# Optimization experiments

Measured on AMD Instinct MI355X. Metric: run time of the kernel, lower is better.

## Reference

```python
import jax, jax.numpy as jnp
import numpy as np

POOL = 7          # pool_size
RES = 42          # ROIS_resolution
CH = 2048         # backbone output channels (Xception)
GCN_DIM = 256     # gcn_outfeat_dim (== gat_outfeat_dim after head split, heads=1)
HEADS = 1
GAT_CH = 256
ALPHA = 0.1       # APPNP teleport
EPS = 1e-3        # keras BatchNormalization epsilon
CHUNKS = CH // GCN_DIM            # 8 channel chunks per ROI
CNODES = CHUNKS * POOL * POOL     # 392 intra-graph nodes


def _rois():
    # fixed ROI boxes (x, y, w, h) on the 42x42 upsampled map:
    # 3x3 grid of 14x14 cells + two horizontal halves + full image
    c = RES // 3
    r = [(x * c, y * c, c, c) for y in range(3) for x in range(3)]
    r += [(0, 0, RES, RES // 2), (0, RES // 2, RES, RES // 2), (0, 0, RES, RES)]
    return r

ROIS = _rois()
NUM_ROIS = len(ROIS)  # 12


def _gcn_adj(n):
    # spektral GCNConv.preprocess on all-ones adjacency: D^-1/2 (A + I) D^-1/2
    a = np.ones((n, n), np.float32) + np.eye(n, dtype=np.float32)
    d = a.sum(1)
    return jnp.asarray(a / np.sqrt(np.outer(d, d)))

A_INTRA = _gcn_adj(CNODES)        # (392, 392)
A_INTER = _gcn_adj(NUM_ROIS + 1)  # (13, 13)


def _appnp(x, a, w, b):
    # APPNPConv, propagations=1, sigmoid MLP: (1-a)*A@m + a*m
    m = jax.nn.sigmoid(x @ w + b)
    return (1.0 - ALPHA) * jnp.einsum('nm,...mf->...nf', a, m) + ALPHA * m


def _gat(x, a, k, a_self, a_neigh, b):
    # GATConv._call_dense (inference: dropout off); a has add_self_loops folded in
    xp = jnp.einsum('...ni,iho->...nho', x, k)          # (...,N,H,C)
    s = jnp.einsum('...nhi,iho->...nho', xp, a_self)    # (...,N,H,1)
    t = jnp.einsum('...nhi,iho->...nho', xp, a_neigh)   # (...,N,H,1)
    coef = s + jnp.swapaxes(t, -3, -1)                  # (...,N,H,N)
    coef = jax.nn.leaky_relu(coef, 0.2)
    mask = jnp.where(a == 0.0, -1e10, 0.0)              # (N,N) (all-connected here)
    coef = jax.nn.softmax(coef + mask[:, None, :], axis=-1)
    out = jnp.einsum('...nhm,...mhi->...nhi', coef, xp)
    out = out.reshape(out.shape[:-2] + (HEADS * GAT_CH,))  # concat heads
    return jax.nn.elu(out + b)


def _gnn_block(x, a, aw, ab, gk, gs, gn, gb):
    h = _appnp(x, a, aw, ab) + x
    return _gat(h, a, gk, gs, gn, gb) + h


def setup_inputs() -> dict:
    key = jax.random.key(0)
    ks = jax.random.split(key, 8)
    s = 0.05
    return {
        'base_out': jax.random.normal(ks[0], (8, POOL, POOL, CH), jnp.float32),
        'appnp_w': jax.random.normal(ks[1], (GCN_DIM, GCN_DIM), jnp.float32) * s,
        'appnp_b': jnp.zeros((GCN_DIM,), jnp.float32),
        'gat_kernel': jax.random.normal(ks[2], (GCN_DIM, HEADS, GAT_CH), jnp.float32) * s,
        'gat_attn_self': jax.random.normal(ks[3], (GAT_CH, HEADS, 1), jnp.float32) * s,
        'gat_attn_neighs': jax.random.normal(ks[4], (GAT_CH, HEADS, 1), jnp.float32) * s,
        'gat_bias': jnp.zeros((HEADS * GAT_CH,), jnp.float32),
        'pool_feat_w': jax.random.normal(ks[5], (GCN_DIM, 2 * GCN_DIM), jnp.float32) * s,
        'pool_feat_b': jnp.zeros((2 * GCN_DIM,), jnp.float32),
        'pool_attn_w': jax.random.normal(ks[6], (GCN_DIM, 2 * GCN_DIM), jnp.float32) * s,
        'pool_attn_b': jnp.zeros((2 * GCN_DIM,), jnp.float32),
        'bn_gamma': jnp.ones((2 * GCN_DIM,), jnp.float32),
        'bn_beta': jnp.zeros((2 * GCN_DIM,), jnp.float32),
        'bn_mean': jnp.zeros((2 * GCN_DIM,), jnp.float32),
        'bn_var': jnp.ones((2 * GCN_DIM,), jnp.float32),
        'dense_w': jax.random.normal(ks[7], (2 * GCN_DIM, 200), jnp.float32) * s,
        'dense_b': jnp.zeros((200,), jnp.float32),
    }


def reference(base_out, appnp_w, appnp_b, gat_kernel, gat_attn_self, gat_attn_neighs,
              gat_bias, pool_feat_w, pool_feat_b, pool_attn_w, pool_attn_b,
              bn_gamma, bn_beta, bn_mean, bn_var, dense_w, dense_b):
    B = base_out.shape[0]
    # upsample backbone features to ROI resolution
    x0 = jax.image.resize(base_out, (B, RES, RES, CH), 'bilinear')
    # RoiPoolingConv: crop each static ROI and resize to (POOL, POOL)
    pooled = [jax.image.resize(x0[:, y:y + h, x:x + w, :], (B, POOL, POOL, CH), 'bilinear')
              for (x, y, w, h) in ROIS]
    pooled.append(base_out)  # global node (pool_size == base_out spatial dim)
    rois = jnp.stack(pooled, axis=1)  # (B, R+1, 7, 7, CH)
    # _temp_nodes_transform: split channels into CHUNKS, concat along node axis
    nodes = rois.reshape(B, NUM_ROIS + 1, POOL * POOL, CHUNKS, GCN_DIM)
    nodes = nodes.transpose(0, 1, 3, 2, 4).reshape(B, NUM_ROIS + 1, CNODES, GCN_DIM)
    gnn = (appnp_w, appnp_b, gat_kernel, gat_attn_self, gat_attn_neighs, gat_bias)
    # intra-ROI graphs: 13 independent 392-node graphs (batched over (B, R+1))
    x2_intra = _gnn_block(nodes, A_INTRA, *gnn).reshape(B, (NUM_ROIS + 1) * CNODES, GCN_DIM)
    # inter-ROI graphs: 392 independent 13-node graphs
    xt = nodes.transpose(0, 2, 1, 3)  # (B, CNODES, R+1, GCN_DIM)
    x2_inter = _gnn_block(xt, A_INTER, *gnn).reshape(B, CNODES * (NUM_ROIS + 1), GCN_DIM)
    x2 = jnp.concatenate([x2_intra, x2_inter], axis=1)  # (B, 10192, 256)
    # GlobalAttentionPool(512)
    feat = x2 @ pool_feat_w + pool_feat_b
    gate = jax.nn.sigmoid(x2 @ pool_attn_w + pool_attn_b)
    xf = jnp.sum(gate * feat, axis=1)  # (B, 512)
    # BatchNorm (inference) + softmax classifier
    xn = (xf - bn_mean) / jnp.sqrt(bn_var + EPS) * bn_gamma + bn_beta
    return jax.nn.softmax(xn @ dense_w + dense_b, axis=-1)
```

## Files before the change

### kernel.cpp

```cpp
#include <hip/hip_runtime.h>
#include <math.h>


typedef __attribute__((ext_vector_type(8))) short bf16x8;
typedef __attribute__((ext_vector_type(4))) float f32x4;

#define MFMA16x32(a, b, c) __builtin_amdgcn_mfma_f32_16x16x32_bf16((a), (b), (c), 0, 0, 0)

__device__ __forceinline__ float sigmoidf_(float x) { return 1.0f / (1.0f + expf(-x)); }
__device__ __forceinline__ float leakyf_(float x) { return x >= 0.0f ? x : 0.2f * x; }
__device__ __forceinline__ float eluf_(float x) { return x > 0.0f ? x : expm1f(x); }
__device__ __forceinline__ short f2bf(float f) {
  unsigned u = __builtin_bit_cast(unsigned, f);
  unsigned r = u + 0x7fffu + ((u >> 16) & 1u);
  return (short)(r >> 16);
}
__device__ __forceinline__ float bf2f(short s) {
  unsigned u = ((unsigned)(unsigned short)s) << 16;
  return __builtin_bit_cast(float, u);
}
__device__ __forceinline__ f32x4 fzero4() {
  f32x4 z;
  #pragma unroll
  for (int i = 0; i < 4; ++i) z[i] = 0.0f;
  return z;
}

__global__ void wtab_k(float* __restrict__ wtab) {
  const int RX[12] = {0,14,28, 0,14,28, 0,14,28, 0, 0, 0};
  const int RY[12] = {0, 0, 0,14,14,14,28,28,28, 0,21, 0};
  const int RW[12] = {14,14,14,14,14,14,14,14,14,42,42,42};
  const int RH[12] = {14,14,14,14,14,14,14,14,14,21,21,42};
  for (int e = threadIdx.x; e < 13 * 2 * 49; e += blockDim.x) {
    const int roi = e / 98;
    const int rest = e % 98;
    const int axis = rest / 49;
    const int o = (rest % 49) / 7;
    const int ib = rest % 7;
    float wout;
    if (roi == 12) {
      wout = (o == ib) ? 1.0f : 0.0f;
    } else {
      const int start = axis ? RX[roi] : RY[roi];
      const int len = axis ? RW[roi] : RH[roi];
      const float s = (float)len / 7.0f;
      const float oc = (o + 0.5f) * s - 0.5f;
      float wsum = 0.0f, dot = 0.0f;
      for (int j = 0; j < len; ++j) {
        float w = 1.0f - fabsf((float)j - oc) / s;
        if (w <= 0.0f) continue;
        wsum += w;
        const float ic = ((float)(start + j) + 0.5f) / 6.0f - 0.5f;
        const float fl = floorf(ic);
        const int ia = (int)fl;
        const float fr = ic - fl;
        int c0 = ia;     if (c0 < 0) c0 = 0; if (c0 > 6) c0 = 6;
        int c1 = ia + 1; if (c1 < 0) c1 = 0; if (c1 > 6) c1 = 6;
        float u = 0.0f;
        if (c0 == ib) u += 1.0f - fr;
        if (c1 == ib) u += fr;
        dot += w * u;
      }
      wout = dot / wsum;
    }
    wtab[e] = wout;
  }
}

__global__ void wcvt_k(const float* __restrict__ src, short* __restrict__ hi,
                       int K, int N) {
  const int idx = blockIdx.x * 256 + threadIdx.x;
  if (idx >= K * N) return;
  const int k = idx / N, n = idx % N;
  hi[(size_t)n * K + k] = f2bf(src[idx]);
}

__global__ void wcvt_pool_k(const float* __restrict__ Wf, const float* __restrict__ Wa,
                            short* __restrict__ BT) {
  const int idx = blockIdx.x * 256 + threadIdx.x;
  if (idx >= 1024 * 256) return;
  const int n = idx >> 8, k = idx & 255;
  const int p = n >> 4, i = n & 15;
  const int sc = ((p >> 1) << 4) + i;
  const float v = (p & 1) ? Wa[(size_t)k * 512 + sc] : Wf[(size_t)k * 512 + sc];
  BT[(size_t)n * 256 + k] = f2bf(v);
}

__global__ void wvec_k(const float* __restrict__ Wk, const float* __restrict__ as,
                       const float* __restrict__ an, float* __restrict__ was,
                       float* __restrict__ wan) {
  const int w = threadIdx.x >> 6, l = threadIdx.x & 63;
  const int row = blockIdx.x * 4 + w;
  const float* p = Wk + (size_t)row * 256;
  float s = 0.0f, t = 0.0f;
  #pragma unroll
  for (int j = 0; j < 4; ++j) {
    const int o = l + j * 64;
    const float v = p[o];
    s = fmaf(v, as[o], s);
    t = fmaf(v, an[o], t);
  }
  #pragma unroll
  for (int off = 32; off; off >>= 1) { s += __shfl_down(s, off); t += __shfl_down(t, off); }
  if (l == 0) { was[row] = s; wan[row] = t; }
}

__global__ __launch_bounds__(256) void nodes_k(const float* __restrict__ base,
                                               const float* __restrict__ wtab,
                                               short* __restrict__ nodes) {
  const int blk = blockIdx.x;
  const int chunk = blk & 7;
  const int br = blk >> 3;
  const int r = br % 13;
  const int b = br / 13;
  const int f = threadIdx.x;
  __shared__ float W49[49][50];
  const float* wv = wtab + (r * 2 + 0) * 49;
  const float* wh = wtab + (r * 2 + 1) * 49;
  for (int e = f; e < 2401; e += 256) {
    const int o = e / 49, in = e % 49;
    W49[o][in] = wv[(o / 7) * 7 + in / 7] * wh[(o % 7) * 7 + in % 7];
  }
  __syncthreads();
  float bv[49];
  const float* bp = base + (size_t)b * 49 * 2048 + chunk * 256 + f;
  #pragma unroll
  for (int in = 0; in < 49; ++in) bv[in] = bp[(size_t)in * 2048];
  const size_t obase = ((size_t)(b * 13 + r) * 392 + chunk * 49) * 256 + f;
  for (int o = 0; o < 49; ++o) {
    float acc = 0.0f;
    #pragma unroll
    for (int in = 0; in < 49; ++in) acc = fmaf(W49[o][in], bv[in], acc);
    nodes[obase + (size_t)o * 256] = f2bf(acc);
  }
}

enum { EP_PLAIN = 0, EP_SIG = 1, EP_POOL = 3 };

template <int EPI>
__global__ __launch_bounds__(256) void gemm_t(
    const short* __restrict__ A, const short* __restrict__ BT,
    const int Kpad, const int nkt, const int Mvalid,
    const float* __restrict__ e0, const float* __restrict__ e1,
    short* __restrict__ Cs, float* __restrict__ xf) {
  const int tid = threadIdx.x;
  const int w = tid >> 6, l = tid & 63;
  const int lr = l & 15, kb = l >> 4;
  const int wr = w >> 1, wc = w & 1;

  int row0, col0, rbase = 0, bseg = 0;
  if constexpr (EPI == EP_POOL) {
    const int bid = blockIdx.x;
    const int eff = (bid & 7) * 640 + (bid >> 3);
    const int mt = eff >> 3, ct = eff & 7;
    row0 = mt * 128; col0 = ct * 128;
    rbase = (mt % 40) * 128;
    bseg = (mt / 40) & 7;
  } else {
    row0 = blockIdx.x * 128; col0 = blockIdx.y * 128;
  }

  __shared__ short As[128][32];
  __shared__ short Bs[128][32];

  const int srow = w * 32 + (l >> 2);
  const int sso = (l & 3) * 8;
  const short* ag0 = A + (size_t)(row0 + srow) * Kpad + sso;
  const short* ag1 = ag0 + (size_t)16 * Kpad;
  const short* bg0 = BT + (size_t)(col0 + srow) * Kpad + sso;
  const short* bg1 = bg0 + (size_t)16 * Kpad;

  f32x4 acc[4][4];
  #pragma unroll
  for (int i = 0; i < 4; ++i)
    #pragma unroll
    for (int j = 0; j < 4; ++j) acc[i][j] = fzero4();

  bf16x8 ra0 = *(const bf16x8*)ag0;
  bf16x8 ra1 = *(const bf16x8*)ag1;
  bf16x8 rb0 = *(const bf16x8*)bg0;
  bf16x8 rb1 = *(const bf16x8*)bg1;

  for (int kt = 0; kt < nkt; ++kt) {
    __syncthreads();
    *(bf16x8*)&As[srow][sso] = ra0;
    *(bf16x8*)&As[srow + 16][sso] = ra1;
    *(bf16x8*)&Bs[srow][sso] = rb0;
    *(bf16x8*)&Bs[srow + 16][sso] = rb1;
    if (kt + 1 < nkt) {
      const int ko = (kt + 1) * 32;
      ra0 = *(const bf16x8*)(ag0 + ko);
      ra1 = *(const bf16x8*)(ag1 + ko);
      rb0 = *(const bf16x8*)(bg0 + ko);
      rb1 = *(const bf16x8*)(bg1 + ko);
    }
    __syncthreads();
    bf16x8 va[4], vb[4];
    #pragma unroll
    for (int i = 0; i < 4; ++i) va[i] = *(const bf16x8*)&As[wr * 64 + i * 16 + lr][kb * 8];
    #pragma unroll
    for (int j = 0; j < 4; ++j) vb[j] = *(const bf16x8*)&Bs[wc * 64 + j * 16 + lr][kb * 8];
    #pragma unroll
    for (int i = 0; i < 4; ++i)
      #pragma unroll
      for (int j = 0; j < 4; ++j) acc[i][j] = MFMA16x32(va[i], vb[j], acc[i][j]);
  }

  if constexpr (EPI == EP_PLAIN || EPI == EP_SIG) {
    #pragma unroll
    for (int j = 0; j < 4; ++j) {
      const int col = col0 + wc * 64 + j * 16 + lr;
      float bs = 0.0f;
      if constexpr (EPI == EP_SIG) bs = e0[col];
      #pragma unroll
      for (int i = 0; i < 4; ++i) {
        const int row = row0 + wr * 64 + i * 16 + kb * 4;
        #pragma unroll
        for (int r = 0; r < 4; ++r) {
          if (row + r < Mvalid) {
            float o = acc[i][j][r];
            if constexpr (EPI == EP_SIG) o = sigmoidf_(o + bs);
            Cs[(size_t)(row + r) * 256 + col] = f2bf(o);
          }
        }
      }
    }
  } else {
    #pragma unroll
    for (int jp = 0; jp < 2; ++jp) {
      const int j = jp * 2;
      const int cg = col0 + wc * 64 + j * 16;
      const int realcol = ((cg >> 5) << 4) + lr;
      const float bfv = e0[realcol], bav = e1[realcol];
      float cs = 0.0f;
      #pragma unroll
      for (int i = 0; i < 4; ++i) {
        const int rl = rbase + wr * 64 + i * 16 + kb * 4;
        #pragma unroll
        for (int r = 0; r < 4; ++r) {
          if (rl + r < 5096) {
            const float fv = acc[i][j][r] + bfv;
            const float gv = acc[i][j + 1][r] + bav;
            cs += sigmoidf_(gv) * fv;
          }
        }
      }
      cs += __shfl_xor(cs, 16);
      cs += __shfl_xor(cs, 32);
      if (l < 16) atomicAdd(&xf[(size_t)bseg * 512 + realcol], cs);
    }
  }
}

__global__ __launch_bounds__(256) void pv_flash_k(
    const short* __restrict__ xpT, const float* __restrict__ sb,
    const float* __restrict__ tb, const float* __restrict__ dinv,
    const float* __restrict__ bias, const short* __restrict__ h,
    short* __restrict__ x2) {
  const int g = blockIdx.z;
  const int rh = blockIdx.y;
  const int ct = blockIdx.x;
  const int tid = threadIdx.x;
  const int w = tid >> 6, l = tid & 63;
  const int lr = l & 15, kb = l >> 4;
  const int wr = w >> 1, wc = w & 1;

  __shared__ short As[128][32];
  __shared__ short Bs[128][32];
  __shared__ float t_s[416];
  __shared__ float red[256];

  for (int i = tid; i < 416; i += 256)
    t_s[i] = (i < 392) ? tb[(size_t)g * 392 + i] : -1e30f;
  __syncthreads();
  float lm = -1e30f;
  for (int i = tid; i < 392; i += 256) lm = fmaxf(lm, t_s[i]);
  red[tid] = lm;
  __syncthreads();
  for (int off = 128; off; off >>= 1) {
    if (tid < off) red[tid] = fmaxf(red[tid], red[tid + off]);
    __syncthreads();
  }
  const float tmax = red[0];

  const int srow = w * 32 + (l >> 2);
  const int sso = (l & 3) * 8;
  const short* bg0 = xpT + ((size_t)g * 256 + ct * 128 + srow) * 448 + sso;
  const short* bg1 = bg0 + (size_t)16 * 448;
  const int bb = g / 13, rr = g % 13;

  for (int rt = 0; rt < 2; ++rt) {
    const int row0 = rh * 256 + rt * 128;
    const int ar0 = row0 + srow, ar1 = row0 + srow + 16;
    const bool v0 = ar0 < 392, v1 = ar1 < 392;
    const float sv0 = v0 ? sb[(size_t)g * 392 + ar0] : 0.0f;
    const float sv1 = v1 ? sb[(size_t)g * 392 + ar1] : 0.0f;
    const float lt0 = leakyf_(sv0 + tmax);
    const float lt1 = leakyf_(sv1 + tmax);

    f32x4 acc[4][4];
    #pragma unroll
    for (int i = 0; i < 4; ++i)
      #pragma unroll
      for (int j = 0; j < 4; ++j) acc[i][j] = fzero4();

    bf16x8 rb0 = *(const bf16x8*)bg0;
    bf16x8 rb1 = *(const bf16x8*)bg1;

    for (int kt = 0; kt < 13; ++kt) {
      __syncthreads();
      *(bf16x8*)&Bs[srow][sso] = rb0;
      *(bf16x8*)&Bs[srow + 16][sso] = rb1;
      {
        const int mb = kt * 32 + sso;
        bf16x8 e0v, e1v;
        #pragma unroll
        for (int i = 0; i < 8; ++i) {
          const float tm = t_s[mb + i];
          e0v[i] = v0 ? f2bf(__expf(leakyf_(sv0 + tm) - lt0)) : (short)0;
          e1v[i] = v1 ? f2bf(__expf(leakyf_(sv1 + tm) - lt1)) : (short)0;
        }
        *(bf16x8*)&As[srow][sso] = e0v;
        *(bf16x8*)&As[srow + 16][sso] = e1v;
      }
      if (kt + 1 < 13) {
        const int ko = (kt + 1) * 32;
        rb0 = *(const bf16x8*)(bg0 + ko);
        rb1 = *(const bf16x8*)(bg1 + ko);
      }
      __syncthreads();
      bf16x8 va[4], vb[4];
      #pragma unroll
      for (int i = 0; i < 4; ++i) va[i] = *(const bf16x8*)&As[wr * 64 + i * 16 + lr][kb * 8];
      #pragma unroll
      for (int j = 0; j < 4; ++j) vb[j] = *(const bf16x8*)&Bs[wc * 64 + j * 16 + lr][kb * 8];
      #pragma unroll
      for (int i = 0; i < 4; ++i)
        #pragma unroll
        for (int j = 0; j < 4; ++j) acc[i][j] = MFMA16x32(va[i], vb[j], acc[i][j]);
    }

    #pragma unroll
    for (int j = 0; j < 4; ++j) {
      const int col = ct * 128 + wc * 64 + j * 16 + lr;
      const float bv = bias[col];
      #pragma unroll
      for (int i = 0; i < 4; ++i) {
        const int rl = row0 + wr * 64 + i * 16 + kb * 4;
        #pragma unroll
        for (int r = 0; r < 4; ++r) {
          const int row = rl + r;
          if (row < 392) {
            const size_t grow = (size_t)g * 392 + row;
            const float o = acc[i][j][r] * dinv[grow];
            const float val = eluf_(o + bv) + bf2f(h[grow * 256 + col]);
            x2[((size_t)bb * 5120 + rr * 392 + row) * 256 + col] = f2bf(val);
          }
        }
      }
    }
  }
}

__global__ __launch_bounds__(256) void denom_k(const float* __restrict__ sb,
    const float* __restrict__ tb, float* __restrict__ dinv) {
  const int g = blockIdx.x;
  const int tid = threadIdx.x;
  __shared__ float t_s[392];
  __shared__ float red[256];
  for (int i = tid; i < 392; i += 256) t_s[i] = tb[(size_t)g * 392 + i];
  __syncthreads();
  float lm = -1e30f;
  for (int i = tid; i < 392; i += 256) lm = fmaxf(lm, t_s[i]);
  red[tid] = lm;
  __syncthreads();
  for (int off = 128; off; off >>= 1) {
    if (tid < off) red[tid] = fmaxf(red[tid], red[tid + off]);
    __syncthreads();
  }
  const float tmax = red[0];
  for (int n = tid; n < 392; n += 256) {
    const float sv = sb[(size_t)g * 392 + n];
    const float lt = leakyf_(sv + tmax);
    float d0 = 0.0f, d1 = 0.0f;
    for (int m = 0; m < 392; m += 2) {
      d0 += __expf(leakyf_(sv + t_s[m]) - lt);
      d1 += __expf(leakyf_(sv + t_s[m + 1]) - lt);
    }
    dinv[(size_t)g * 392 + n] = 1.0f / (d0 + d1);
  }
}

__global__ __launch_bounds__(256) void transpose_k(const short* __restrict__ xp,
                                                   short* __restrict__ xpT) {
  const int m0 = blockIdx.x * 64;
  const int f0 = blockIdx.y * 64;
  const int g = blockIdx.z;
  const int tid = threadIdx.x;
  __shared__ short tile[64][66];
  const int c = tid & 63;
  const int r4 = tid >> 6;
  #pragma unroll
  for (int p = 0; p < 16; ++p) {
    const int row = p * 4 + r4;
    const int m = m0 + row;
    tile[row][c] = (m < 392) ? xp[((size_t)g * 392 + m) * 256 + f0 + c] : (short)0;
  }
  __syncthreads();
  #pragma unroll
  for (int p = 0; p < 16; ++p) {
    const int fr = p * 4 + r4;
    xpT[((size_t)g * 256 + f0 + fr) * 448 + m0 + c] = tile[c][fr];
  }
}

__global__ void sums_intra_k(const short* __restrict__ m, float* __restrict__ S) {
  const int g = blockIdx.x;
  const int f = threadIdx.x;
  const short* p = m + (size_t)g * 392 * 256 + f;
  float a0 = 0.0f, a1 = 0.0f, a2 = 0.0f, a3 = 0.0f;
  for (int c = 0; c < 392; c += 4) {
    a0 += bf2f(p[(size_t)(c + 0) * 256]);
    a1 += bf2f(p[(size_t)(c + 1) * 256]);
    a2 += bf2f(p[(size_t)(c + 2) * 256]);
    a3 += bf2f(p[(size_t)(c + 3) * 256]);
  }
  S[(size_t)g * 256 + f] = (a0 + a1) + (a2 + a3);
}

__global__ void sums_inter_k(const short* __restrict__ m, float* __restrict__ S) {
  const int g = blockIdx.x;
  const int b = g / 392, c = g % 392;
  const int f = threadIdx.x;
  const short* p = m + ((size_t)(b * 13) * 392 + c) * 256 + f;
  float acc = 0.0f;
  #pragma unroll
  for (int r = 0; r < 13; ++r) acc += bf2f(p[(size_t)r * 392 * 256]);
  S[(size_t)g * 256 + f] = acc;
}

template <int INTRA>
__global__ void h_st_v(const short* __restrict__ nodes, const short* __restrict__ m,
                       const float* __restrict__ S, const float* __restrict__ was,
                       const float* __restrict__ wan, short* __restrict__ h,
                       float* __restrict__ sb, float* __restrict__ tb) {
  const int row = blockIdx.x * 8 + (threadIdx.x >> 5);
  const int f0 = (threadIdx.x & 31) * 8;
  int g;
  float inv;
  if constexpr (INTRA) { g = row / 392; inv = 1.0f / 393.0f; }
  else { const int b = row / 5096; g = b * 392 + row % 392; inv = 1.0f / 14.0f; }
  const size_t e0 = (size_t)row * 256 + f0;
  const bf16x8 mv8 = *(const bf16x8*)(m + e0);
  const bf16x8 nv8 = *(const bf16x8*)(nodes + e0);
  const float* Sp = S + (size_t)g * 256 + f0;
  bf16x8 o;
  float s = 0.0f, t = 0.0f;
  #pragma unroll
  for (int i = 0; i < 8; ++i) {
    const float mv = bf2f(mv8[i]);
    const float hv = 0.9f * (Sp[i] + mv) * inv + 0.1f * mv + bf2f(nv8[i]);
    o[i] = f2bf(hv);
    s = fmaf(hv, was[f0 + i], s);
    t = fmaf(hv, wan[f0 + i], t);
  }
  *(bf16x8*)(h + e0) = o;
  #pragma unroll
  for (int off = 16; off; off >>= 1) {
    s += __shfl_xor(s, off, 32);
    t += __shfl_xor(t, off, 32);
  }
  if ((threadIdx.x & 31) == 0) { sb[row] = s; tb[row] = t; }
}

__global__ __launch_bounds__(256) void attn_inter_k(const short* __restrict__ xp,
    const float* __restrict__ sb, const float* __restrict__ tb,
    const short* __restrict__ h, const float* __restrict__ bias,
    short* __restrict__ x2, int B) {
  const int g = blockIdx.x;
  const int b = g / 392, c = g % 392;
  const int tid = threadIdx.x;
  __shared__ float xps[13][256];
  __shared__ float e_s[13][14];
  __shared__ float sv[13], tv[13], denom[13];
  __shared__ float tmax_s;
  for (int lin = tid; lin < 13 * 256; lin += 256) {
    const int r = lin >> 8, f = lin & 255;
    xps[r][f] = bf2f(xp[((size_t)(b * 13 + r) * 392 + c) * 256 + f]);
  }
  if (tid < 13) {
    const size_t row = (size_t)(b * 13 + tid) * 392 + c;
    sv[tid] = sb[row];
    tv[tid] = tb[row];
  }
  __syncthreads();
  if (tid == 0) {
    float mx = tv[0];
    for (int r = 1; r < 13; ++r) mx = fmaxf(mx, tv[r]);
    tmax_s = mx;
  }
  __syncthreads();
  if (tid < 169) {
    const int n = tid / 13, mm = tid % 13;
    e_s[n][mm] = expf(leakyf_(sv[n] + tv[mm]) - leakyf_(sv[n] + tmax_s));
  }
  __syncthreads();
  if (tid < 13) {
    float d = 0.0f;
    for (int mm = 0; mm < 13; ++mm) d += e_s[tid][mm];
    denom[tid] = d;
  }
  __syncthreads();
  const int f = tid;
  for (int n = 0; n < 13; ++n) {
    float acc = 0.0f;
    #pragma unroll
    for (int mm = 0; mm < 13; ++mm) acc = fmaf(e_s[n][mm], xps[mm][f], acc);
    const float o = acc / denom[n];
    const size_t hbase = ((size_t)(b * 13 + n) * 392 + c) * 256 + f;
    x2[(((size_t)(B + b)) * 5120 + (size_t)n * 392 + c) * 256 + f] =
        f2bf(eluf_(o + bias[f]) + bf2f(h[hbase]));
  }
}

__global__ __launch_bounds__(256) void head_k(const float* __restrict__ xf,
    const float* __restrict__ gamma, const float* __restrict__ beta,
    const float* __restrict__ mean, const float* __restrict__ var,
    const float* __restrict__ Wd, const float* __restrict__ bd,
    float* __restrict__ out) {
  const int b = blockIdx.x;
  const int tid = threadIdx.x;
  __shared__ float xn[512];
  __shared__ float red[256];
  for (int i = tid; i < 512; i += 256) {
    const float v = xf[(size_t)b * 512 + i];
    xn[i] = (v - mean[i]) / sqrtf(var[i] + 1e-3f) * gamma[i] + beta[i];
  }
  __syncthreads();
  float logit = -1e30f;
  if (tid < 200) {
    float acc = bd[tid];
    for (int i = 0; i < 512; ++i) acc = fmaf(xn[i], Wd[(size_t)i * 200 + tid], acc);
    logit = acc;
  }
  red[tid] = logit;
  __syncthreads();
  for (int off = 128; off; off >>= 1) {
    if (tid < off) red[tid] = fmaxf(red[tid], red[tid + off]);
    __syncthreads();
  }
  const float mx = red[0];
  __syncthreads();
  const float e = (tid < 200) ? expf(logit - mx) : 0.0f;
  red[tid] = e;
  __syncthreads();
  for (int off = 128; off; off >>= 1) {
    if (tid < off) red[tid] += red[tid + off];
    __syncthreads();
  }
  const float inv = 1.0f / red[0];
  if (tid < 200) out[(size_t)b * 200 + tid] = e * inv;
}

extern "C" void kernel_launch(void* const* d_in, const int* in_sizes, int n_in,
                              void* d_out, int out_size, void* d_ws, size_t ws_size,
                              hipStream_t stream) {
  (void)n_in; (void)out_size; (void)ws_size;
  const float* base    = (const float*)d_in[0];
  const float* appnp_w = (const float*)d_in[1];
  const float* appnp_b = (const float*)d_in[2];
  const float* gat_k   = (const float*)d_in[3];
  const float* gat_as  = (const float*)d_in[4];
  const float* gat_an  = (const float*)d_in[5];
  const float* gat_b   = (const float*)d_in[6];
  const float* pf_w    = (const float*)d_in[7];
  const float* pf_b    = (const float*)d_in[8];
  const float* pa_w    = (const float*)d_in[9];
  const float* pa_b    = (const float*)d_in[10];
  const float* bn_g    = (const float*)d_in[11];
  const float* bn_be   = (const float*)d_in[12];
  const float* bn_mu   = (const float*)d_in[13];
  const float* bn_va   = (const float*)d_in[14];
  const float* dw      = (const float*)d_in[15];
  const float* db      = (const float*)d_in[16];
  float* out = (float*)d_out;

  const int B = in_sizes[0] / (49 * 2048);
  const int G = B * 13;
  const int R = G * 392;
  const int Mt = (R + 127) / 128;
  const int Rpad = Mt * 128;
  const int MP = 2 * B * 5120;

  char* ws = (char*)d_ws;
  size_t off = 0;
  auto alloc = [&](size_t bytes) -> void* {
    void* p = (void*)(ws + off);
    off += (bytes + 255) & ~(size_t)255;
    return p;
  };
  float* wtab   = (float*)alloc((size_t)13 * 2 * 49 * 4);
  short* aWhi   = (short*)alloc((size_t)256 * 256 * 2);
  short* gkhi   = (short*)alloc((size_t)256 * 256 * 2);
  short* pwcomb = (short*)alloc((size_t)1024 * 256 * 2);
  float* was    = (float*)alloc((size_t)256 * 4);
  float* wan    = (float*)alloc((size_t)256 * 4);
  short* nodes  = (short*)alloc((size_t)Rpad * 256 * 2);
  short* mbuf   = (short*)alloc((size_t)R * 256 * 2);
  short* hbuf   = (short*)alloc((size_t)Rpad * 256 * 2);
  short* xpbuf  = (short*)alloc((size_t)R * 256 * 2);
  short* xpT    = (short*)alloc((size_t)G * 256 * 448 * 2);
  short* x2buf  = (short*)alloc((size_t)MP * 256 * 2);
  float* Sintra = (float*)alloc((size_t)G * 256 * 4);
  float* Sinter = (float*)alloc((size_t)B * 392 * 256 * 4);
  float* sbuf   = (float*)alloc((size_t)R * 4);
  float* tbuf   = (float*)alloc((size_t)R * 4);
  float* dinv   = (float*)alloc((size_t)R * 4);
  float* xf     = (float*)alloc((size_t)B * 512 * 4);

  hipMemsetAsync(xf, 0, (size_t)B * 512 * 4, stream);
  wtab_k<<<1, 256, 0, stream>>>(wtab);
  wcvt_k<<<(256 * 256 + 255) / 256, 256, 0, stream>>>(appnp_w, aWhi, 256, 256);
  wcvt_k<<<(256 * 256 + 255) / 256, 256, 0, stream>>>(gat_k, gkhi, 256, 256);
  wcvt_pool_k<<<1024, 256, 0, stream>>>(pf_w, pa_w, pwcomb);
  wvec_k<<<64, 256, 0, stream>>>(gat_k, gat_as, gat_an, was, wan);
  nodes_k<<<B * 13 * 8, 256, 0, stream>>>(base, wtab, nodes);

  gemm_t<EP_SIG><<<dim3(Mt, 2), 256, 0, stream>>>(nodes, aWhi, 256, 8, R,
      appnp_b, nullptr, mbuf, nullptr);
  sums_intra_k<<<G, 256, 0, stream>>>(mbuf, Sintra);
  sums_inter_k<<<B * 392, 256, 0, stream>>>(mbuf, Sinter);

  h_st_v<1><<<R / 8, 256, 0, stream>>>(nodes, mbuf, Sintra, was, wan, hbuf, sbuf, tbuf);
  gemm_t<EP_PLAIN><<<dim3(Mt, 2), 256, 0, stream>>>(hbuf, gkhi, 256, 8, R,
      nullptr, nullptr, xpbuf, nullptr);
  transpose_k<<<dim3(7, 4, G), 256, 0, stream>>>(xpbuf, xpT);
  denom_k<<<G, 256, 0, stream>>>(sbuf, tbuf, dinv);
  pv_flash_k<<<dim3(2, 2, G), 256, 0, stream>>>(xpT, sbuf, tbuf, dinv, gat_b,
                                                hbuf, x2buf);

  h_st_v<0><<<R / 8, 256, 0, stream>>>(nodes, mbuf, Sinter, was, wan, hbuf, sbuf, tbuf);
  gemm_t<EP_PLAIN><<<dim3(Mt, 2), 256, 0, stream>>>(hbuf, gkhi, 256, 8, R,
      nullptr, nullptr, xpbuf, nullptr);
  attn_inter_k<<<B * 392, 256, 0, stream>>>(xpbuf, sbuf, tbuf, hbuf, gat_b, x2buf, B);

  gemm_t<EP_POOL><<<5120, 256, 0, stream>>>(x2buf, pwcomb, 256, 8, 0,
      pf_b, pa_b, nullptr, xf);
  head_k<<<B, 256, 0, stream>>>(xf, bn_g, bn_be, bn_mu, bn_va, dw, db, out);
}
```

Before: 418.3 us.

## Replace dense intra-ROI GAT attention with sorted-sweep factorized softmax

The 392x392 GAT attention (transpose, denominator and MFMA flash kernels) is replaced by one kernel that exploits the rank-1 structure of leaky_relu(s_i + t_j). Nodes are sorted by t and by -s, and a single merged sweep keeps prefix sums of exp(t) and exp(0.2 t) weighted by xp. Each output row is then formed from two exponential factors in O(N) rather than O(N^2). The intra-ROI column sums are also split into partial and final reduction kernels to expose more parallelism. In exchange the kernel carries an O(N^2) per-thread ranking loop, is serial over the 392 nodes per thread, and runs only 2*G blocks of 128 threads, which limits occupancy.

```diff
diff --git a/kernel.cpp b/kernel.cpp
--- a/kernel.cpp
+++ b/kernel.cpp
@@ -252,180 +252,156 @@
   }
 }
 
-__global__ __launch_bounds__(256) void pv_flash_k(
-    const short* __restrict__ xpT, const float* __restrict__ sb,
-    const float* __restrict__ tb, const float* __restrict__ dinv,
-    const float* __restrict__ bias, const short* __restrict__ h,
-    short* __restrict__ x2) {
-  const int g = blockIdx.z;
-  const int rh = blockIdx.y;
-  const int ct = blockIdx.x;
+__global__ __launch_bounds__(128) void attn_sweep_k(
+    const short* __restrict__ xp, const float* __restrict__ sb,
+    const float* __restrict__ tb, const float* __restrict__ bias,
+    const short* __restrict__ h, short* __restrict__ x2) {
+  const int g = blockIdx.y;
+  const int f = blockIdx.x * 128 + threadIdx.x;
   const int tid = threadIdx.x;
-  const int w = tid >> 6, l = tid & 63;
-  const int lr = l & 15, kb = l >> 4;
-  const int wr = w >> 1, wc = w & 1;
-
-  __shared__ short As[128][32];
-  __shared__ short Bs[128][32];
-  __shared__ float t_s[416];
-  __shared__ float red[256];
-
-  for (int i = tid; i < 416; i += 256)
-    t_s[i] = (i < 392) ? tb[(size_t)g * 392 + i] : -1e30f;
+  __shared__ float t_s[392], s_s[392], u_s[392], v_s[392];
+  __shared__ unsigned short p_s[392], pp_s[392];
+  __shared__ unsigned short evt_s[784];
+  __shared__ float red[128];
+  const size_t gbase = (size_t)g * 392;
+  for (int i = tid; i < 392; i += 128) {
+    t_s[i] = tb[gbase + i];
+    s_s[i] = sb[gbase + i];
+  }
   __syncthreads();
   float lm = -1e30f;
-  for (int i = tid; i < 392; i += 256) lm = fmaxf(lm, t_s[i]);
+  for (int i = tid; i < 392; i += 128) lm = fmaxf(lm, t_s[i]);
   red[tid] = lm;
   __syncthreads();
-  for (int off = 128; off; off >>= 1) {
+  for (int off = 64; off; off >>= 1) {
     if (tid < off) red[tid] = fmaxf(red[tid], red[tid + off]);
     __syncthreads();
   }
   const float tmax = red[0];
 
-  const int srow = w * 32 + (l >> 2);
-  const int sso = (l & 3) * 8;
-  const short* bg0 = xpT + ((size_t)g * 256 + ct * 128 + srow) * 448 + sso;
-  const short* bg1 = bg0 + (size_t)16 * 448;
-  const int bb = g / 13, rr = g % 13;
-
-  for (int rt = 0; rt < 2; ++rt) {
-    const int row0 = rh * 256 + rt * 128;
-    const int ar0 = row0 + srow, ar1 = row0 + srow + 16;
-    const bool v0 = ar0 < 392, v1 = ar1 < 392;
-    const float sv0 = v0 ? sb[(size_t)g * 392 + ar0] : 0.0f;
-    const float sv1 = v1 ? sb[(size_t)g * 392 + ar1] : 0.0f;
-    const float lt0 = leakyf_(sv0 + tmax);
-    const float lt1 = leakyf_(sv1 + tmax);
-
-    f32x4 acc[4][4];
-    #pragma unroll
-    for (int i = 0; i < 4; ++i)
+  int rt_l[4], rs_l[4];
+  #pragma unroll
+  for (int q = 0; q < 4; ++q) {
+    const int i = tid + q * 128;
+    rt_l[q] = -1; rs_l[q] = -1;
+    if (i < 392) {
+      const float ti = t_s[i], si = s_s[i];
+      u_s[i] = __expf(ti - tmax);
+      v_s[i] = __expf(0.2f * (ti - tmax));
+      int rt = 0, rs = 0, p = 0;
+      for (int jj = 0; jj < 392; ++jj) {
+        const float tj = t_s[jj], sj = s_s[jj];
+        rt += (int)((tj < ti) | ((tj == ti) & (jj < i)));
+        rs += (int)((sj > si) | ((sj == si) & (jj < i)));
+        p  += (int)(tj < -si);
+      }
+      rt_l[q] = rt; rs_l[q] = rs;
+      p_s[i] = (unsigned short)p;
+      pp_s[rs] = (unsigned short)p;
+      evt_s[p + rs] = (unsigned short)(0x8000u | i);
+    }
+  }
+  __syncthreads();
+  #pragma unroll
+  for (int q = 0; q < 4; ++q) {
+    const int i = tid + q * 128;
+    if (i < 392) {
+      const int rt = rt_l[q];
+      int lo = 0, hi = 392;
+      while (lo < hi) {
+        const int mid = (lo + hi) >> 1;
+        if ((int)pp_s[mid] <= rt) lo = mid + 1; else hi = mid;
+      }
+      evt_s[rt + lo] = (unsigned short)i;
+    }
+  }
+  __syncthreads();
+
+  float U1 = 0.0f;
+  for (int i = 0; i < 392; ++i) U1 += u_s[i];
+  const short* xg = xp + gbase * 256 + f;
+  const short* hg = h + gbase * 256 + f;
+  float T1a = 0.0f, T1b = 0.0f, T1c = 0.0f, T1d = 0.0f;
+  for (int i = 0; i < 392; i += 4) {
+    T1a += u_s[i + 0] * bf2f(xg[(size_t)(i + 0) * 256]);
+    T1b += u_s[i + 1] * bf2f(xg[(size_t)(i + 1) * 256]);
+    T1c += u_s[i + 2] * bf2f(xg[(size_t)(i + 2) * 256]);
+    T1d += u_s[i + 3] * bf2f(xg[(size_t)(i + 3) * 256]);
+  }
+  const float T1 = (T1a + T1b) + (T1c + T1d);
+
+  const int bb2 = g / 13, rr2 = g % 13;
+  short* x2g = x2 + ((size_t)bb2 * 5120 + (size_t)rr2 * 392) * 256 + f;
+  const float bf_ = bias[f];
+  float P1 = 0.0f, P2 = 0.0f, p1s = 0.0f, p2s = 0.0f;
+
+  auto loadfor = [&](int e) -> short {
+    const unsigned ev = evt_s[e];
+    const size_t row = ev & 0x7FFFu;
+    return (ev & 0x8000u) ? hg[row * 256] : xg[row * 256];
+  };
+  auto process = [&](int e, short xv) {
+    const unsigned ev = evt_s[e];
+    const int row = (int)(ev & 0x7FFFu);
+    const float x = bf2f(xv);
+    if (!(ev & 0x8000u)) {
+      const float uu = u_s[row], vv = v_s[row];
+      P1 = fmaf(uu, x, P1); P2 = fmaf(vv, x, P2);
+      p1s += uu; p2s += vv;
+    } else {
+      const float z = s_s[row] + tmax;
+      const float c1 = (z < 0.0f) ? __expf(0.8f * z) : 1.0f;
+      const float c2 = (z < 0.0f) ? 1.0f : __expf(-0.8f * z);
+      const float num = c1 * (T1 - P1) + c2 * P2;
+      const float den = c1 * (U1 - p1s) + c2 * p2s;
+      const float val = eluf_(num / den + bf_) + x;
+      x2g[(size_t)row * 256] = f2bf(val);
+    }
+  };
+
+  short bufA[16], bufB[16];
+  #pragma unroll
+  for (int q = 0; q < 16; ++q) bufA[q] = loadfor(q);
+  for (int bat = 0; bat < 49; bat += 2) {
+    if (bat + 1 < 49) {
       #pragma unroll
-      for (int j = 0; j < 4; ++j) acc[i][j] = fzero4();
-
-    bf16x8 rb0 = *(const bf16x8*)bg0;
-    bf16x8 rb1 = *(const bf16x8*)bg1;
-
-    for (int kt = 0; kt < 13; ++kt) {
-      __syncthreads();
-      *(bf16x8*)&Bs[srow][sso] = rb0;
-      *(bf16x8*)&Bs[srow + 16][sso] = rb1;
-      {
-        const int mb = kt * 32 + sso;
-        bf16x8 e0v, e1v;
+      for (int q = 0; q < 16; ++q) bufB[q] = loadfor((bat + 1) * 16 + q);
+    }
+    #pragma unroll
+    for (int q = 0; q < 16; ++q) process(bat * 16 + q, bufA[q]);
+    if (bat + 1 < 49) {
+      if (bat + 2 < 49) {
         #pragma unroll
-        for (int i = 0; i < 8; ++i) {
-          const float tm = t_s[mb + i];
-          e0v[i] = v0 ? f2bf(__expf(leakyf_(sv0 + tm) - lt0)) : (short)0;
-          e1v[i] = v1 ? f2bf(__expf(leakyf_(sv1 + tm) - lt1)) : (short)0;
-        }
-        *(bf16x8*)&As[srow][sso] = e0v;
-        *(bf16x8*)&As[srow + 16][sso] = e1v;
+        for (int q = 0; q < 16; ++q) bufA[q] = loadfor((bat + 2) * 16 + q);
       }
-      if (kt + 1 < 13) {
-        const int ko = (kt + 1) * 32;
-        rb0 = *(const bf16x8*)(bg0 + ko);
-        rb1 = *(const bf16x8*)(bg1 + ko);
-      }
-      __syncthreads();
-      bf16x8 va[4], vb[4];
       #pragma unroll
-      for (int i = 0; i < 4; ++i) va[i] = *(const bf16x8*)&As[wr * 64 + i * 16 + lr][kb * 8];
-      #pragma unroll
-      for (int j = 0; j < 4; ++j) vb[j] = *(const bf16x8*)&Bs[wc * 64 + j * 16 + lr][kb * 8];
-      #pragma unroll
-      for (int i = 0; i < 4; ++i)
-        #pragma unroll
-        for (int j = 0; j < 4; ++j) acc[i][j] = MFMA16x32(va[i], vb[j], acc[i][j]);
-    }
-
-    #pragma unroll
-    for (int j = 0; j < 4; ++j) {
-      const int col = ct * 128 + wc * 64 + j * 16 + lr;
-      const float bv = bias[col];
-      #pragma unroll
-      for (int i = 0; i < 4; ++i) {
-        const int rl = row0 + wr * 64 + i * 16 + kb * 4;
-        #pragma unroll
-        for (int r = 0; r < 4; ++r) {
-          const int row = rl + r;
-          if (row < 392) {
-            const size_t grow = (size_t)g * 392 + row;
-            const float o = acc[i][j][r] * dinv[grow];
-            const float val = eluf_(o + bv) + bf2f(h[grow * 256 + col]);
-            x2[((size_t)bb * 5120 + rr * 392 + row) * 256 + col] = f2bf(val);
-          }
-        }
-      }
-    }
-  }
-}
-
-__global__ __launch_bounds__(256) void denom_k(const float* __restrict__ sb,
-    const float* __restrict__ tb, float* __restrict__ dinv) {
-  const int g = blockIdx.x;
-  const int tid = threadIdx.x;
-  __shared__ float t_s[392];
-  __shared__ float red[256];
-  for (int i = tid; i < 392; i += 256) t_s[i] = tb[(size_t)g * 392 + i];
-  __syncthreads();
-  float lm = -1e30f;
-  for (int i = tid; i < 392; i += 256) lm = fmaxf(lm, t_s[i]);
-  red[tid] = lm;
-  __syncthreads();
-  for (int off = 128; off; off >>= 1) {
-    if (tid < off) red[tid] = fmaxf(red[tid], red[tid + off]);
-    __syncthreads();
-  }
-  const float tmax = red[0];
-  for (int n = tid; n < 392; n += 256) {
-    const float sv = sb[(size_t)g * 392 + n];
-    const float lt = leakyf_(sv + tmax);
-    float d0 = 0.0f, d1 = 0.0f;
-    for (int m = 0; m < 392; m += 2) {
-      d0 += __expf(leakyf_(sv + t_s[m]) - lt);
-      d1 += __expf(leakyf_(sv + t_s[m + 1]) - lt);
-    }
-    dinv[(size_t)g * 392 + n] = 1.0f / (d0 + d1);
-  }
-}
-
-__global__ __launch_bounds__(256) void transpose_k(const short* __restrict__ xp,
-                                                   short* __restrict__ xpT) {
-  const int m0 = blockIdx.x * 64;
-  const int f0 = blockIdx.y * 64;
-  const int g = blockIdx.z;
-  const int tid = threadIdx.x;
-  __shared__ short tile[64][66];
-  const int c = tid & 63;
-  const int r4 = tid >> 6;
-  #pragma unroll
-  for (int p = 0; p < 16; ++p) {
-    const int row = p * 4 + r4;
-    const int m = m0 + row;
-    tile[row][c] = (m < 392) ? xp[((size_t)g * 392 + m) * 256 + f0 + c] : (short)0;
-  }
-  __syncthreads();
-  #pragma unroll
-  for (int p = 0; p < 16; ++p) {
-    const int fr = p * 4 + r4;
-    xpT[((size_t)g * 256 + f0 + fr) * 448 + m0 + c] = tile[c][fr];
-  }
-}
-
-__global__ void sums_intra_k(const short* __restrict__ m, float* __restrict__ S) {
-  const int g = blockIdx.x;
+      for (int q = 0; q < 16; ++q) process((bat + 1) * 16 + q, bufB[q]);
+    }
+  }
+}
+
+__global__ void sums_intra_part_k(const short* __restrict__ m, float* __restrict__ Sp) {
+  const int g = blockIdx.x >> 3, ch = blockIdx.x & 7;
   const int f = threadIdx.x;
-  const short* p = m + (size_t)g * 392 * 256 + f;
+  const short* p = m + ((size_t)g * 392 + ch * 49) * 256 + f;
   float a0 = 0.0f, a1 = 0.0f, a2 = 0.0f, a3 = 0.0f;
-  for (int c = 0; c < 392; c += 4) {
+  for (int c = 0; c < 48; c += 4) {
     a0 += bf2f(p[(size_t)(c + 0) * 256]);
     a1 += bf2f(p[(size_t)(c + 1) * 256]);
     a2 += bf2f(p[(size_t)(c + 2) * 256]);
     a3 += bf2f(p[(size_t)(c + 3) * 256]);
   }
-  S[(size_t)g * 256 + f] = (a0 + a1) + (a2 + a3);
+  a0 += bf2f(p[(size_t)48 * 256]);
+  Sp[((size_t)g * 8 + ch) * 256 + f] = (a0 + a1) + (a2 + a3);
+}
+
+__global__ void sums_intra_fin_k(const float* __restrict__ Sp, float* __restrict__ S) {
+  const int g = blockIdx.x;
+  const int f = threadIdx.x;
+  float acc = 0.0f;
+  #pragma unroll
+  for (int ch = 0; ch < 8; ++ch) acc += Sp[((size_t)g * 8 + ch) * 256 + f];
+  S[(size_t)g * 256 + f] = acc;
 }
 
 __global__ void sums_inter_k(const short* __restrict__ m, float* __restrict__ S) {
@@ -609,13 +585,12 @@
   short* mbuf   = (short*)alloc((size_t)R * 256 * 2);
   short* hbuf   = (short*)alloc((size_t)Rpad * 256 * 2);
   short* xpbuf  = (short*)alloc((size_t)R * 256 * 2);
-  short* xpT    = (short*)alloc((size_t)G * 256 * 448 * 2);
   short* x2buf  = (short*)alloc((size_t)MP * 256 * 2);
+  float* Spart  = (float*)alloc((size_t)G * 8 * 256 * 4);
   float* Sintra = (float*)alloc((size_t)G * 256 * 4);
   float* Sinter = (float*)alloc((size_t)B * 392 * 256 * 4);
   float* sbuf   = (float*)alloc((size_t)R * 4);
   float* tbuf   = (float*)alloc((size_t)R * 4);
-  float* dinv   = (float*)alloc((size_t)R * 4);
   float* xf     = (float*)alloc((size_t)B * 512 * 4);
 
   hipMemsetAsync(xf, 0, (size_t)B * 512 * 4, stream);
@@ -628,16 +603,14 @@
 
   gemm_t<EP_SIG><<<dim3(Mt, 2), 256, 0, stream>>>(nodes, aWhi, 256, 8, R,
       appnp_b, nullptr, mbuf, nullptr);
-  sums_intra_k<<<G, 256, 0, stream>>>(mbuf, Sintra);
+  sums_intra_part_k<<<G * 8, 256, 0, stream>>>(mbuf, Spart);
+  sums_intra_fin_k<<<G, 256, 0, stream>>>(Spart, Sintra);
   sums_inter_k<<<B * 392, 256, 0, stream>>>(mbuf, Sinter);
 
   h_st_v<1><<<R / 8, 256, 0, stream>>>(nodes, mbuf, Sintra, was, wan, hbuf, sbuf, tbuf);
   gemm_t<EP_PLAIN><<<dim3(Mt, 2), 256, 0, stream>>>(hbuf, gkhi, 256, 8, R,
       nullptr, nullptr, xpbuf, nullptr);
-  transpose_k<<<dim3(7, 4, G), 256, 0, stream>>>(xpbuf, xpT);
-  denom_k<<<G, 256, 0, stream>>>(sbuf, tbuf, dinv);
-  pv_flash_k<<<dim3(2, 2, G), 256, 0, stream>>>(xpT, sbuf, tbuf, dinv, gat_b,
-                                                hbuf, x2buf);
+  attn_sweep_k<<<dim3(2, G), 128, 0, stream>>>(xpbuf, sbuf, tbuf, gat_b, hbuf, x2buf);
 
   h_st_v<0><<<R / 8, 256, 0, stream>>>(nodes, mbuf, Sinter, was, wan, hbuf, sbuf, tbuf);
   gemm_t<EP_PLAIN><<<dim3(Mt, 2), 256, 0, stream>>>(hbuf, gkhi, 256, 8, R,
```

Measured after the change: 540.3 us. 1.29x slower.
